# Optimization experiments

Measured on AMD Instinct MI355X. Metric: run time of the kernel, lower is better.

The kernel has to match this reference:

```python
import jax, jax.numpy as jnp
import numpy as np

B, T, H, NH = 4, 1024, 1024, 16
HS = H // NH
FF = 4 * H
EPS = 1e-5


def setup_inputs() -> dict:
    key = jax.random.key(0)
    ks = jax.random.split(key, 12)
    s = 0.02
    inp = {
        "x": jax.random.normal(ks[0], (B, T, H), jnp.float32),
        # attention projections, stored as [in, out] so y = x @ W + b
        "Wq": jax.random.normal(ks[1], (H, H), jnp.float32) * s,
        "bq": jnp.zeros((H,), jnp.float32),
        "Wk": jax.random.normal(ks[2], (H, H), jnp.float32) * s,
        "bk": jnp.zeros((H,), jnp.float32),
        "Wv": jax.random.normal(ks[3], (H, H), jnp.float32) * s,
        "bv": jnp.zeros((H,), jnp.float32),
        "Wo": jax.random.normal(ks[4], (H, H), jnp.float32) * s,
        "bo": jnp.zeros((H,), jnp.float32),
        # layernorms
        "ln1_w": jnp.ones((H,), jnp.float32),
        "ln1_b": jnp.zeros((H,), jnp.float32),
        "ln2_w": jnp.ones((H,), jnp.float32),
        "ln2_b": jnp.zeros((H,), jnp.float32),
        # MLP
        "Wfc": jax.random.normal(ks[5], (H, FF), jnp.float32) * s,
        "bfc": jnp.zeros((FF,), jnp.float32),
        "Wpr": jax.random.normal(ks[6], (FF, H), jnp.float32) * s,
        "bpr": jnp.zeros((H,), jnp.float32),
    }
    return inp


def _layernorm(x, w, b):
    mu = jnp.mean(x, axis=-1, keepdims=True)
    var = jnp.mean(jnp.square(x - mu), axis=-1, keepdims=True)
    return (x - mu) * jax.lax.rsqrt(var + EPS) * w + b


def _rope(x):
    # x: [B, nh, T, hs]; interleaved-pair RoPE, base 10000
    half = HS // 2
    inv_freq = 1.0 / (10000.0 ** (jnp.arange(half, dtype=jnp.float32) / half))
    ang = jnp.arange(T, dtype=jnp.float32)[:, None] * inv_freq[None, :]  # [T, half]
    cos, sin = jnp.cos(ang), jnp.sin(ang)
    xr = x.reshape(*x.shape[:-1], half, 2)
    x0, x1 = xr[..., 0], xr[..., 1]
    r0 = x0 * cos - x1 * sin
    r1 = x0 * sin + x1 * cos
    return jnp.stack([r0, r1], axis=-1).reshape(x.shape)


def _block(x, Wq, bq, Wk, bk, Wv, bv, Wo, bo, ln1_w, ln1_b, ln2_w, ln2_b, Wfc, bfc, Wpr, bpr):
    # --- attention sub-block ---
    h1 = _layernorm(x, ln1_w, ln1_b)
    q = (h1 @ Wq + bq).reshape(B, T, NH, HS).transpose(0, 2, 1, 3)  # [B,nh,T,hs]
    k = (h1 @ Wk + bk).reshape(B, T, NH, HS).transpose(0, 2, 1, 3)
    v = (h1 @ Wv + bv).reshape(B, T, NH, HS).transpose(0, 2, 1, 3)
    q, k = _rope(q), _rope(k)
    scores = jnp.einsum('bhqd,bhkd->bhqk', q, k) / jnp.sqrt(jnp.float32(HS))
    attn = jax.nn.softmax(scores, axis=-1)
    # NOTE: original applies the causal mask AFTER softmax (multiplicative, no renorm)
    causal = jnp.tril(jnp.ones((T, T), jnp.float32))[None, None]
    attn = attn * causal
    out = jnp.einsum('bhqk,bhkd->bhqd', attn, v)
    out = out.transpose(0, 2, 1, 3).reshape(B, T, H)
    x = x + (out @ Wo + bo)
    # --- MLP sub-block ---
    h2 = _layernorm(x, ln2_w, ln2_b)
    m = jax.nn.gelu(h2 @ Wfc + bfc, approximate=False)
    x = x + (m @ Wpr + bpr)
    return x


def reference(x, Wq, bq, Wk, bk, Wv, bv, Wo, bo, ln1_w, ln1_b, ln2_w, ln2_b, Wfc, bfc, Wpr, bpr):
    return _block(x, Wq, bq, Wk, bk, Wv, bv, Wo, bo, ln1_w, ln1_b, ln2_w, ln2_b, Wfc, bfc, Wpr, bpr)
```

## Files before the change

### kernel.cpp

```cpp
#include <hip/hip_runtime.h>
#include <hip/hip_bf16.h>

typedef unsigned short u16;
typedef __attribute__((ext_vector_type(8))) short bf16x8;
typedef __attribute__((ext_vector_type(4))) float f32x4;
typedef __attribute__((ext_vector_type(4))) unsigned short u16x4;

#define B_  4
#define T_  1024
#define H_  1024
#define NH_ 16
#define HS_ 64
#define FF_ 4096
#define M_  (B_*T_)
#define QKV_S 3072

__device__ __forceinline__ u16 f2bf(float f){
  union { float f; unsigned u; } v; v.f = f;
  unsigned r = v.u + 0x7fffu + ((v.u >> 16) & 1u);
  return (u16)(r >> 16);
}
__device__ __forceinline__ float bf2f(u16 h){
  union { unsigned u; float f; } v; v.u = ((unsigned)h) << 16;
  return v.f;
}
__device__ __forceinline__ unsigned pack2bf(float a, float b){
  __hip_bfloat162 h = __float22bfloat162_rn(make_float2(a, b));
  union { __hip_bfloat162 h; unsigned u; } c; c.h = h;
  return c.u;
}

__device__ __forceinline__ void gload_lds16(const void* g, void* l){
  __builtin_amdgcn_global_load_lds(
      (const __attribute__((address_space(1))) unsigned int*)g,
      (__attribute__((address_space(3))) unsigned int*)l,
      16, 0, 0);
}

__global__ __launch_bounds__(256) void transpose_cvt(const float* __restrict__ W,
                                                     u16* __restrict__ Wt, int K, int N)
{
  __shared__ u16 tile[64][68];
  const int k0 = blockIdx.y * 64, n0 = blockIdx.x * 64;
  const int tid = threadIdx.x;
  #pragma unroll
  for (int it = 0; it < 4; ++it){
    int ci = tid + it * 256;
    int kr = ci >> 4, nc = ci & 15;
    float4 f = *(const float4*)(W + (size_t)(k0 + kr) * N + n0 + nc * 4);
    tile[kr][nc*4+0] = f2bf(f.x);
    tile[kr][nc*4+1] = f2bf(f.y);
    tile[kr][nc*4+2] = f2bf(f.z);
    tile[kr][nc*4+3] = f2bf(f.w);
  }
  __syncthreads();
  #pragma unroll
  for (int it = 0; it < 4; ++it){
    int co = tid + it * 256;
    int nr = co >> 4, kc = co & 15;
    u16x4 o;
    o[0] = tile[kc*4+0][nr];
    o[1] = tile[kc*4+1][nr];
    o[2] = tile[kc*4+2][nr];
    o[3] = tile[kc*4+3][nr];
    *(u16x4*)(Wt + (size_t)(n0 + nr) * K + k0 + kc * 4) = o;
  }
}

__global__ __launch_bounds__(256) void vtrans_k(const u16* __restrict__ qkv,
                                                u16* __restrict__ vtg)
{
  __shared__ u16 tile[64][72];
  const int bh = blockIdx.y, tt = blockIdx.x * 64;
  const int b = bh >> 4, h = bh & 15;
  const size_t src = (size_t)b * T_ * QKV_S + h * HS_ + 2048;
  const int tid = threadIdx.x;
  #pragma unroll
  for (int it = 0; it < 2; ++it){
    int ci = tid + it * 256;
    int r = ci >> 3, c = ci & 7;
    bf16x8 vvv = *(const bf16x8*)(qkv + src + (size_t)(tt + r) * QKV_S + c * 8);
    *(bf16x8*)&tile[r][c * 8] = vvv;
  }
  __syncthreads();
  #pragma unroll
  for (int it = 0; it < 2; ++it){
    int co = tid + it * 256;
    int d = co >> 3, c = co & 7;
    bf16x8 ov;
    #pragma unroll
    for (int j = 0; j < 8; ++j) ov[j] = (short)tile[c * 8 + j][d];
    *(bf16x8*)(vtg + (size_t)bh * HS_ * T_ + (size_t)d * T_ + tt + c * 8) = ov;
  }
}

__global__ void concat3_k(const float* __restrict__ a, const float* __restrict__ b,
                          const float* __restrict__ c, float* __restrict__ o){
  int i = blockIdx.x * 256 + threadIdx.x;
  if (i >= QKV_S) return;
  o[i] = (i < 1024) ? a[i] : (i < 2048) ? b[i - 1024] : c[i - 2048];
}

__global__ void rope_table_k(float* __restrict__ tab){
  int i = blockIdx.x * blockDim.x + threadIdx.x;
  if (i >= T_ * 32) return;
  int t = i >> 5, f = i & 31;
  float inv = powf(10000.0f, -(float)f * (1.0f / 32.0f));
  float ang = (float)t * inv;
  tab[i*2+0] = cosf(ang);
  tab[i*2+1] = sinf(ang);
}

__global__ void rope_apply_k(u16* __restrict__ qkv, const float* __restrict__ tab){
  int i = blockIdx.x * blockDim.x + threadIdx.x;
  if (i >= B_*T_*NH_*32) return;
  int pr = i & 31;
  int nh = (i >> 5) & (NH_ - 1);
  int bt = i >> 9;
  int t  = bt & (T_ - 1);
  size_t idx = (size_t)bt * QKV_S + nh * HS_ + pr * 2;
  float c = tab[(t*32 + pr)*2], s = tab[(t*32 + pr)*2 + 1];
  {
    float x0 = bf2f(qkv[idx]), x1 = bf2f(qkv[idx+1]);
    qkv[idx]   = f2bf((x0 * c - x1 * s) * 0.125f);
    qkv[idx+1] = f2bf((x0 * s + x1 * c) * 0.125f);
  }
  {
    float x0 = bf2f(qkv[idx+1024]), x1 = bf2f(qkv[idx+1025]);
    qkv[idx+1024] = f2bf(x0 * c - x1 * s);
    qkv[idx+1025] = f2bf(x0 * s + x1 * c);
  }
}

__global__ __launch_bounds__(256) void ln_kernel(const float* __restrict__ x,
    const float* __restrict__ w, const float* __restrict__ bgain,
    u16* __restrict__ out)
{
  const int row = blockIdx.x;
  const int t = threadIdx.x;
  float4 vv = ((const float4*)(x + (size_t)row * H_))[t];
  float s  = vv.x + vv.y + vv.z + vv.w;
  float s2 = vv.x*vv.x + vv.y*vv.y + vv.z*vv.z + vv.w*vv.w;
  #pragma unroll
  for (int mm = 1; mm < 64; mm <<= 1){ s += __shfl_xor(s, mm); s2 += __shfl_xor(s2, mm); }
  __shared__ float red[8];
  int wid = t >> 6;
  if ((t & 63) == 0){ red[wid] = s; red[4 + wid] = s2; }
  __syncthreads();
  s  = red[0] + red[1] + red[2] + red[3];
  s2 = red[4] + red[5] + red[6] + red[7];
  float mu  = s * (1.0f / H_);
  float var = s2 * (1.0f / H_) - mu * mu;
  float rin = rsqrtf(var + 1e-5f);
  float4 wv = ((const float4*)w)[t];
  float4 bv = ((const float4*)bgain)[t];
  u16x4 ov;
  ov[0] = f2bf((vv.x - mu) * rin * wv.x + bv.x);
  ov[1] = f2bf((vv.y - mu) * rin * wv.y + bv.y);
  ov[2] = f2bf((vv.z - mu) * rin * wv.z + bv.z);
  ov[3] = f2bf((vv.w - mu) * rin * wv.w + bv.w);
  ((u16x4*)(out + (size_t)row * H_))[t] = ov;
}

template<int EPI>
__global__ __launch_bounds__(256) void gemm_kernel(
    const u16* __restrict__ A, const u16* __restrict__ Bt,
    const float* __restrict__ bias, const float* __restrict__ res,
    void* __restrict__ Cout, int M, int N, int K)
{
  __shared__ __attribute__((aligned(16))) u16 As[4][128 * 32];
  __shared__ __attribute__((aligned(16))) u16 Bs[4][128 * 32];
  const int tid  = threadIdx.x;
  const int lane = tid & 63;
  const int wid  = tid >> 6;
  const int wm = wid >> 1, wn = wid & 1;
  const int lrow = lane & 15, lkg = lane >> 4;

  const int gx  = gridDim.x;
  const int nwg = gx * gridDim.y;
  const int wg  = blockIdx.y * gx + blockIdx.x;
  const int nx  = nwg >> 3;
  const int swz = (wg & 7) * nx + (wg >> 3);
  const int m0 = (swz / gx) * 128, n0 = (swz % gx) * 128;

  const int srow = tid >> 2;
  const int sdc  = tid & 3;
  const int scs  = sdc ^ ((srow >> 1) & 3);

  const u16* Arow0 = A  + (size_t)(m0 + srow) * K + scs * 8;
  const u16* Brow0 = Bt + (size_t)(n0 + srow) * K + scs * 8;
  const u16* Arow1 = Arow0 + (size_t)64 * K;
  const u16* Brow1 = Brow0 + (size_t)64 * K;
  const int d0 = (srow * 4 + sdc) * 8;
  const int d1 = ((srow + 64) * 4 + sdc) * 8;

  f32x4 acc[4][4] = {};

  const int NT = K >> 5;

  #pragma unroll
  for (int s = 0; s < 3; ++s){
    if (s < NT){
      int k0 = s << 5;
      gload_lds16(Arow0 + k0, &As[s][d0]);
      gload_lds16(Brow0 + k0, &Bs[s][d0]);
      gload_lds16(Arow1 + k0, &As[s][d1]);
      gload_lds16(Brow1 + k0, &Bs[s][d1]);
    }
  }

  for (int t = 0; t < NT; ++t){
    int ahead = NT - 1 - t;
    if (ahead >= 2)      asm volatile("s_waitcnt vmcnt(8)" ::: "memory");
    else if (ahead == 1) asm volatile("s_waitcnt vmcnt(4)" ::: "memory");
    else                 asm volatile("s_waitcnt vmcnt(0)" ::: "memory");
    __builtin_amdgcn_s_barrier();
    __builtin_amdgcn_sched_barrier(0);

    const u16* Asc = As[t & 3];
    const u16* Bsc = Bs[t & 3];
    bf16x8 af[4], bfr[4];
    #pragma unroll
    for (int mi = 0; mi < 4; ++mi){
      int r = wm*64 + mi*16 + lrow;
      af[mi] = *(const bf16x8*)&Asc[(r*4 + (lkg ^ ((r >> 1) & 3))) * 8];
    }
    #pragma unroll
    for (int ni = 0; ni < 4; ++ni){
      int r = wn*64 + ni*16 + lrow;
      bfr[ni] = *(const bf16x8*)&Bsc[(r*4 + (lkg ^ ((r >> 1) & 3))) * 8];
    }
    asm volatile("s_waitcnt lgkmcnt(0)" ::: "memory");
    __builtin_amdgcn_sched_barrier(0);
    __builtin_amdgcn_s_barrier();
    __builtin_amdgcn_sched_barrier(0);

    if (t + 3 < NT){
      int k0 = (t + 3) << 5;
      int sl = (t + 3) & 3;
      gload_lds16(Arow0 + k0, &As[sl][d0]);
      gload_lds16(Brow0 + k0, &Bs[sl][d0]);
      gload_lds16(Arow1 + k0, &As[sl][d1]);
      gload_lds16(Brow1 + k0, &Bs[sl][d1]);
    }

    #pragma unroll
    for (int mi = 0; mi < 4; ++mi)
      #pragma unroll
      for (int ni = 0; ni < 4; ++ni)
        acc[mi][ni] = __builtin_amdgcn_mfma_f32_16x16x32_bf16(af[mi], bfr[ni], acc[mi][ni], 0, 0, 0);
  }

  #pragma unroll
  for (int mi = 0; mi < 4; ++mi){
    #pragma unroll
    for (int ni = 0; ni < 4; ++ni){
      int col = n0 + wn*64 + ni*16 + lrow;
      float bv = bias[col];
      #pragma unroll
      for (int r = 0; r < 4; ++r){
        int row = m0 + wm*64 + mi*16 + lkg*4 + r;
        float v = acc[mi][ni][r] + bv;
        if (EPI == 1){
          v = 0.5f * v * (1.0f + erff(v * 0.70710678118f));
        }
        if (EPI == 2){
          ((float*)Cout)[(size_t)row * N + col] = v + res[(size_t)row * N + col];
        } else {
          ((u16*)Cout)[(size_t)row * N + col] = f2bf(v);
        }
      }
    }
  }
}

__global__ __launch_bounds__(256) void attn_kernel(
    const u16* __restrict__ qkv, const u16* __restrict__ vtg,
    u16* __restrict__ out)
{
  __shared__ u16 K_lds[2][64 * 64];
  __shared__ u16 VT_lds[2][64 * 64];
  __shared__ u16 P_lds[4][16 * 64];
  const int tid = threadIdx.x, lane = tid & 63, w = tid >> 6;
  const int lrow = lane & 15, lkg = lane >> 4;
  const int q0 = blockIdx.x * 64;
  const int bh = blockIdx.y, b = bh >> 4, h = bh & 15;
  const size_t baseq  = (size_t)b * T_ * QKV_S + h * HS_;
  const size_t basek  = baseq + 1024;
  const size_t basevt = (size_t)bh * HS_ * T_;
  const size_t baseo  = (size_t)b * T_ * H_ + h * HS_;
  const int qg = q0 + w * 16 + lrow;

  bf16x8 qa[2];
  {
    const u16* qp = qkv + baseq + (size_t)qg * QKV_S + lkg * 8;
    qa[0] = *(const bf16x8*)qp;
    qa[1] = *(const bf16x8*)(qp + 32);
  }

  const int ci0 = tid, ci1 = tid + 256;
  const int r0 = ci0 >> 3, c0 = ci0 & 7, g0 = c0 ^ (r0 & 7);
  const int r1 = ci1 >> 3, c1 = ci1 & 7, g1 = c1 ^ (r1 & 7);
  const u16* kap0 = qkv + basek + (size_t)r0 * QKV_S + g0 * 8;
  const u16* kap1 = qkv + basek + (size_t)r1 * QKV_S + g1 * 8;
  const u16* vap0 = vtg + basevt + (size_t)r0 * T_ + g0 * 8;
  const u16* vap1 = vtg + basevt + (size_t)r1 * T_ + g1 * 8;
  const int kd0 = ci0 * 8, kd1 = ci1 * 8;

  f32x4 o[4] = {};
  float mrun = -1e30f, lrun = 0.f;

  gload_lds16(kap0, &K_lds[0][kd0]);
  gload_lds16(kap1, &K_lds[0][kd1]);
  gload_lds16(vap0, &VT_lds[0][kd0]);
  gload_lds16(vap1, &VT_lds[0][kd1]);

  int cur = 0;
  for (int t = 0; t < 16; ++t){
    const int kt = t << 6;
    __syncthreads();
    if (t + 1 < 16){
      const size_t ko = (size_t)(t + 1) * 64 * QKV_S;
      gload_lds16(kap0 + ko, &K_lds[cur^1][kd0]);
      gload_lds16(kap1 + ko, &K_lds[cur^1][kd1]);
      if (((t + 1) << 6) <= q0 + 63){
        const int vo = (t + 1) * 64;
        gload_lds16(vap0 + vo, &VT_lds[cur^1][kd0]);
        gload_lds16(vap1 + vo, &VT_lds[cur^1][kd1]);
      }
    }

    f32x4 s[4];
    #pragma unroll
    for (int mi = 0; mi < 4; ++mi){
      f32x4 c = {};
      #pragma unroll
      for (int ss = 0; ss < 2; ++ss){
        int r = mi * 16 + lrow;
        int off = r * 128 + (((ss * 4 + lkg) ^ (r & 7)) * 16);
        bf16x8 kb = *(const bf16x8*)((const char*)K_lds[cur] + off);
        c = __builtin_amdgcn_mfma_f32_16x16x32_bf16(kb, qa[ss], c, 0, 0, 0);
      }
      s[mi] = c;
    }

    float mt = fmaxf(fmaxf(fmaxf(s[0][0], s[0][1]), fmaxf(s[0][2], s[0][3])),
                     fmaxf(fmaxf(s[1][0], s[1][1]), fmaxf(s[1][2], s[1][3])));
    mt = fmaxf(mt, fmaxf(fmaxf(fmaxf(s[2][0], s[2][1]), fmaxf(s[2][2], s[2][3])),
                         fmaxf(fmaxf(s[3][0], s[3][1]), fmaxf(s[3][2], s[3][3]))));
    mt = fmaxf(mt, __shfl_xor(mt, 16));
    mt = fmaxf(mt, __shfl_xor(mt, 32));
    float mnew = fmaxf(mrun, mt);
    float fsc = __expf(mrun - mnew);
    mrun = mnew;

    float p[16];
    float ls = 0.f;
    #pragma unroll
    for (int mi = 0; mi < 4; ++mi){
      #pragma unroll
      for (int r = 0; r < 4; ++r){
        int key = kt + mi * 16 + lkg * 4 + r;
        float pv = __expf(s[mi][r] - mnew);
        ls += pv;
        p[mi * 4 + r] = (key <= qg) ? pv : 0.f;
      }
    }
    ls += __shfl_xor(ls, 16);
    ls += __shfl_xor(ls, 32);
    lrun = lrun * fsc + ls;
    #pragma unroll
    for (int nf = 0; nf < 4; ++nf){
      #pragma unroll
      for (int r = 0; r < 4; ++r) o[nf][r] *= fsc;
    }

    if (kt <= q0 + w * 16 + 15){
      char* pbase = (char*)&P_lds[w][0];
      const int rx = (lrow & 7) << 4;
      #pragma unroll
      for (int mi = 0; mi < 4; ++mi){
        uint2 pk;
        pk.x = pack2bf(p[mi*4+0], p[mi*4+1]);
        pk.y = pack2bf(p[mi*4+2], p[mi*4+3]);
        *(uint2*)(pbase + (lrow * 128 + ((mi * 32 + lkg * 8) ^ rx))) = pk;
      }
      #pragma unroll
      for (int ss = 0; ss < 2; ++ss){
        bf16x8 pb = *(const bf16x8*)(pbase + (lrow * 128 + ((ss * 64 + lkg * 16) ^ rx)));
        #pragma unroll
        for (int nfd = 0; nfd < 4; ++nfd){
          int d = nfd * 16 + lrow;
          int off = d * 128 + (((ss * 4 + lkg) ^ (d & 7)) * 16);
          bf16x8 vb = *(const bf16x8*)((const char*)VT_lds[cur] + off);
          o[nfd] = __builtin_amdgcn_mfma_f32_16x16x32_bf16(vb, pb, o[nfd], 0, 0, 0);
        }
      }
    }
    cur ^= 1;
  }

  float rl = 1.0f / lrun;
  #pragma unroll
  for (int nfd = 0; nfd < 4; ++nfd){
    uint2 ov;
    ov.x = pack2bf(o[nfd][0] * rl, o[nfd][1] * rl);
    ov.y = pack2bf(o[nfd][2] * rl, o[nfd][3] * rl);
    *(uint2*)(out + baseo + (size_t)qg * H_ + nfd * 16 + lkg * 4) = ov;
  }
}

extern "C" void kernel_launch(void* const* d_in, const int* in_sizes, int n_in,
                              void* d_out, int out_size, void* d_ws, size_t ws_size,
                              hipStream_t stream)
{
  (void)in_sizes; (void)n_in; (void)out_size; (void)ws_size;
  const float* x    = (const float*)d_in[0];
  const float* Wq   = (const float*)d_in[1];
  const float* bq   = (const float*)d_in[2];
  const float* Wk   = (const float*)d_in[3];
  const float* bk   = (const float*)d_in[4];
  const float* Wv   = (const float*)d_in[5];
  const float* bv   = (const float*)d_in[6];
  const float* Wo   = (const float*)d_in[7];
  const float* bo   = (const float*)d_in[8];
  const float* ln1w = (const float*)d_in[9];
  const float* ln1b = (const float*)d_in[10];
  const float* ln2w = (const float*)d_in[11];
  const float* ln2b = (const float*)d_in[12];
  const float* Wfc  = (const float*)d_in[13];
  const float* bfc  = (const float*)d_in[14];
  const float* Wpr  = (const float*)d_in[15];
  const float* bpr  = (const float*)d_in[16];

  char* ws = (char*)d_ws;
  u16*  WqkvT = (u16*)(ws + ((size_t) 0 << 20));
  u16*  WoT   = (u16*)(ws + ((size_t) 6 << 20));
  u16*  WfcT  = (u16*)(ws + ((size_t) 8 << 20));
  u16*  WprT  = (u16*)(ws + ((size_t)16 << 20));
  u16*  h1    = (u16*)(ws + ((size_t)24 << 20));
  u16*  qkvb  = (u16*)(ws + ((size_t)32 << 20));
  float* x1   = (float*)(ws + ((size_t)32 << 20));
  u16*  h2    = (u16*)(ws + ((size_t)48 << 20));
  float* bqkv = (float*)(ws + ((size_t)56 << 20));
  float* rtab = (float*)(ws + ((size_t)56 << 20) + (64 << 10));
  u16*  vtg   = (u16*)(ws + ((size_t)57 << 20));
  u16*  mb    = (u16*)(ws + ((size_t)56 << 20));
  u16*  attnout = h1;

  dim3 blk(256);

  transpose_cvt<<<dim3(H_/64,  H_/64),  blk, 0, stream>>>(Wq,  WqkvT,                 H_,  H_);
  transpose_cvt<<<dim3(H_/64,  H_/64),  blk, 0, stream>>>(Wk,  WqkvT + (size_t)1024*1024, H_,  H_);
  transpose_cvt<<<dim3(H_/64,  H_/64),  blk, 0, stream>>>(Wv,  WqkvT + (size_t)2048*1024, H_,  H_);
  transpose_cvt<<<dim3(H_/64,  H_/64),  blk, 0, stream>>>(Wo,  WoT,  H_,  H_);
  transpose_cvt<<<dim3(FF_/64, H_/64),  blk, 0, stream>>>(Wfc, WfcT, H_,  FF_);
  transpose_cvt<<<dim3(H_/64,  FF_/64), blk, 0, stream>>>(Wpr, WprT, FF_, H_);
  concat3_k<<<dim3((QKV_S+255)/256), blk, 0, stream>>>(bq, bk, bv, bqkv);
  rope_table_k<<<dim3((T_*32)/256), blk, 0, stream>>>(rtab);

  ln_kernel<<<dim3(M_), blk, 0, stream>>>(x, ln1w, ln1b, h1);
  gemm_kernel<0><<<dim3(QKV_S/128, M_/128), blk, 0, stream>>>(h1, WqkvT, bqkv, nullptr, qkvb, M_, QKV_S, H_);
  rope_apply_k<<<dim3((B_*T_*NH_*32)/256), blk, 0, stream>>>(qkvb, rtab);
  vtrans_k<<<dim3(T_/64, B_*NH_), blk, 0, stream>>>(qkvb, vtg);
  attn_kernel<<<dim3(T_/64, B_*NH_), blk, 0, stream>>>(qkvb, vtg, attnout);
  gemm_kernel<2><<<dim3(H_/128, M_/128), blk, 0, stream>>>(attnout, WoT, bo, x, x1, M_, H_, H_);
  ln_kernel<<<dim3(M_), blk, 0, stream>>>(x1, ln2w, ln2b, h2);
  gemm_kernel<1><<<dim3(FF_/128, M_/128), blk, 0, stream>>>(h2, WfcT, bfc, nullptr, mb, M_, FF_, H_);
  gemm_kernel<2><<<dim3(H_/128, M_/128), blk, 0, stream>>>(mb, WprT, bpr, x1, (float*)d_out, M_, H_, FF_);
}
```

Before: 290.1 us.

## Restructure GEMM and attention LDS rings to drop per-iteration second barrier

The GEMM becomes templated on ring depth. Stage refills are issued right after the single barrier into the slot consumed in the previous iteration, which removes the second barrier and lgkmcnt wait per K step. A 3-deep ring is used for the wide-N GEMMs (lower LDS, possibly higher occupancy) and a 6-deep ring for the N=1024 GEMMs (more loads in flight). Attention moves from double to triple buffering with prefetch distance two, and now always loads V tiles, even for fully masked tiles where the old code skipped them. Safety of the single barrier depends on the ring depth exceeding the prefetch distance.

```diff
diff --git a/kernel.cpp b/kernel.cpp
--- a/kernel.cpp
+++ b/kernel.cpp
@@ -162,14 +162,14 @@
   ((u16x4*)(out + (size_t)row * H_))[t] = ov;
 }
 
-template<int EPI>
+template<int EPI, int RING>
 __global__ __launch_bounds__(256) void gemm_kernel(
     const u16* __restrict__ A, const u16* __restrict__ Bt,
     const float* __restrict__ bias, const float* __restrict__ res,
     void* __restrict__ Cout, int M, int N, int K)
 {
-  __shared__ __attribute__((aligned(16))) u16 As[4][128 * 32];
-  __shared__ __attribute__((aligned(16))) u16 Bs[4][128 * 32];
+  __shared__ __attribute__((aligned(16))) u16 As[RING][128 * 32];
+  __shared__ __attribute__((aligned(16))) u16 Bs[RING][128 * 32];
   const int tid  = threadIdx.x;
   const int lane = tid & 63;
   const int wid  = tid >> 6;
@@ -195,30 +195,48 @@
   const int d1 = ((srow + 64) * 4 + sdc) * 8;
 
   f32x4 acc[4][4] = {};
-
   const int NT = K >> 5;
-
-  #pragma unroll
-  for (int s = 0; s < 3; ++s){
-    if (s < NT){
-      int k0 = s << 5;
-      gload_lds16(Arow0 + k0, &As[s][d0]);
-      gload_lds16(Brow0 + k0, &Bs[s][d0]);
-      gload_lds16(Arow1 + k0, &As[s][d1]);
-      gload_lds16(Brow1 + k0, &Bs[s][d1]);
-    }
-  }
-
+  constexpr int DIST = RING - 1;
+
+  #pragma unroll
+  for (int s = 0; s < DIST; ++s){
+    int k0 = s << 5;
+    gload_lds16(Arow0 + k0, &As[s][d0]);
+    gload_lds16(Brow0 + k0, &Bs[s][d0]);
+    gload_lds16(Arow1 + k0, &As[s][d1]);
+    gload_lds16(Brow1 + k0, &Bs[s][d1]);
+  }
+
+  int rs = 0;
+  int wsl = DIST;
   for (int t = 0; t < NT; ++t){
-    int ahead = NT - 1 - t;
-    if (ahead >= 2)      asm volatile("s_waitcnt vmcnt(8)" ::: "memory");
-    else if (ahead == 1) asm volatile("s_waitcnt vmcnt(4)" ::: "memory");
-    else                 asm volatile("s_waitcnt vmcnt(0)" ::: "memory");
+    int cnt = NT - 1 - t; if (cnt > DIST - 1) cnt = DIST - 1;
+    if constexpr (RING == 6){
+      if (cnt >= 4)      asm volatile("s_waitcnt vmcnt(16)" ::: "memory");
+      else if (cnt == 3) asm volatile("s_waitcnt vmcnt(12)" ::: "memory");
+      else if (cnt == 2) asm volatile("s_waitcnt vmcnt(8)"  ::: "memory");
+      else if (cnt == 1) asm volatile("s_waitcnt vmcnt(4)"  ::: "memory");
+      else               asm volatile("s_waitcnt vmcnt(0)"  ::: "memory");
+    } else {
+      if (cnt >= 1)      asm volatile("s_waitcnt vmcnt(4)"  ::: "memory");
+      else               asm volatile("s_waitcnt vmcnt(0)"  ::: "memory");
+    }
     __builtin_amdgcn_s_barrier();
     __builtin_amdgcn_sched_barrier(0);
 
-    const u16* Asc = As[t & 3];
-    const u16* Bsc = Bs[t & 3];
+    if (t + DIST < NT){
+      int k0 = (t + DIST) << 5;
+      gload_lds16(Arow0 + k0, &As[wsl][d0]);
+      gload_lds16(Brow0 + k0, &Bs[wsl][d0]);
+      gload_lds16(Arow1 + k0, &As[wsl][d1]);
+      gload_lds16(Brow1 + k0, &Bs[wsl][d1]);
+    }
+    wsl = (wsl + 1 == RING) ? 0 : wsl + 1;
+
+    const u16* Asc = As[rs];
+    const u16* Bsc = Bs[rs];
+    rs = (rs + 1 == RING) ? 0 : rs + 1;
+
     bf16x8 af[4], bfr[4];
     #pragma unroll
     for (int mi = 0; mi < 4; ++mi){
@@ -230,20 +248,6 @@
       int r = wn*64 + ni*16 + lrow;
       bfr[ni] = *(const bf16x8*)&Bsc[(r*4 + (lkg ^ ((r >> 1) & 3))) * 8];
     }
-    asm volatile("s_waitcnt lgkmcnt(0)" ::: "memory");
-    __builtin_amdgcn_sched_barrier(0);
-    __builtin_amdgcn_s_barrier();
-    __builtin_amdgcn_sched_barrier(0);
-
-    if (t + 3 < NT){
-      int k0 = (t + 3) << 5;
-      int sl = (t + 3) & 3;
-      gload_lds16(Arow0 + k0, &As[sl][d0]);
-      gload_lds16(Brow0 + k0, &Bs[sl][d0]);
-      gload_lds16(Arow1 + k0, &As[sl][d1]);
-      gload_lds16(Brow1 + k0, &Bs[sl][d1]);
-    }
-
     #pragma unroll
     for (int mi = 0; mi < 4; ++mi)
       #pragma unroll
@@ -278,8 +282,8 @@
     const u16* __restrict__ qkv, const u16* __restrict__ vtg,
     u16* __restrict__ out)
 {
-  __shared__ u16 K_lds[2][64 * 64];
-  __shared__ u16 VT_lds[2][64 * 64];
+  __shared__ u16 K_lds[3][64 * 64];
+  __shared__ u16 VT_lds[3][64 * 64];
   __shared__ u16 P_lds[4][16 * 64];
   const int tid = threadIdx.x, lane = tid & 63, w = tid >> 6;
   const int lrow = lane & 15, lkg = lane >> 4;
@@ -310,25 +314,37 @@
   f32x4 o[4] = {};
   float mrun = -1e30f, lrun = 0.f;
 
-  gload_lds16(kap0, &K_lds[0][kd0]);
-  gload_lds16(kap1, &K_lds[0][kd1]);
-  gload_lds16(vap0, &VT_lds[0][kd0]);
-  gload_lds16(vap1, &VT_lds[0][kd1]);
-
-  int cur = 0;
+  #pragma unroll
+  for (int s = 0; s < 2; ++s){
+    const size_t ko = (size_t)s * 64 * QKV_S;
+    const int    vo = s * 64;
+    gload_lds16(kap0 + ko, &K_lds[s][kd0]);
+    gload_lds16(kap1 + ko, &K_lds[s][kd1]);
+    gload_lds16(vap0 + vo, &VT_lds[s][kd0]);
+    gload_lds16(vap1 + vo, &VT_lds[s][kd1]);
+  }
+
+  int rs = 0, wsl = 2;
   for (int t = 0; t < 16; ++t){
     const int kt = t << 6;
-    __syncthreads();
-    if (t + 1 < 16){
-      const size_t ko = (size_t)(t + 1) * 64 * QKV_S;
-      gload_lds16(kap0 + ko, &K_lds[cur^1][kd0]);
-      gload_lds16(kap1 + ko, &K_lds[cur^1][kd1]);
-      if (((t + 1) << 6) <= q0 + 63){
-        const int vo = (t + 1) * 64;
-        gload_lds16(vap0 + vo, &VT_lds[cur^1][kd0]);
-        gload_lds16(vap1 + vo, &VT_lds[cur^1][kd1]);
-      }
-    }
+    if (t < 15) asm volatile("s_waitcnt vmcnt(4)" ::: "memory");
+    else        asm volatile("s_waitcnt vmcnt(0)" ::: "memory");
+    __builtin_amdgcn_s_barrier();
+    __builtin_amdgcn_sched_barrier(0);
+
+    if (t + 2 < 16){
+      const size_t ko = (size_t)(t + 2) * 64 * QKV_S;
+      const int    vo = (t + 2) * 64;
+      gload_lds16(kap0 + ko, &K_lds[wsl][kd0]);
+      gload_lds16(kap1 + ko, &K_lds[wsl][kd1]);
+      gload_lds16(vap0 + vo, &VT_lds[wsl][kd0]);
+      gload_lds16(vap1 + vo, &VT_lds[wsl][kd1]);
+    }
+    wsl = (wsl + 1 == 3) ? 0 : wsl + 1;
+
+    const u16* Kc  = K_lds[rs];
+    const u16* VTc = VT_lds[rs];
+    rs = (rs + 1 == 3) ? 0 : rs + 1;
 
     f32x4 s[4];
     #pragma unroll
@@ -338,7 +354,7 @@
       for (int ss = 0; ss < 2; ++ss){
         int r = mi * 16 + lrow;
         int off = r * 128 + (((ss * 4 + lkg) ^ (r & 7)) * 16);
-        bf16x8 kb = *(const bf16x8*)((const char*)K_lds[cur] + off);
+        bf16x8 kb = *(const bf16x8*)((const char*)Kc + off);
         c = __builtin_amdgcn_mfma_f32_16x16x32_bf16(kb, qa[ss], c, 0, 0, 0);
       }
       s[mi] = c;
@@ -392,12 +408,11 @@
         for (int nfd = 0; nfd < 4; ++nfd){
           int d = nfd * 16 + lrow;
           int off = d * 128 + (((ss * 4 + lkg) ^ (d & 7)) * 16);
-          bf16x8 vb = *(const bf16x8*)((const char*)VT_lds[cur] + off);
+          bf16x8 vb = *(const bf16x8*)((const char*)VTc + off);
           o[nfd] = __builtin_amdgcn_mfma_f32_16x16x32_bf16(vb, pb, o[nfd], 0, 0, 0);
         }
       }
     }
-    cur ^= 1;
   }
 
   float rl = 1.0f / lrun;
@@ -460,12 +475,12 @@
   rope_table_k<<<dim3((T_*32)/256), blk, 0, stream>>>(rtab);
 
   ln_kernel<<<dim3(M_), blk, 0, stream>>>(x, ln1w, ln1b, h1);
-  gemm_kernel<0><<<dim3(QKV_S/128, M_/128), blk, 0, stream>>>(h1, WqkvT, bqkv, nullptr, qkvb, M_, QKV_S, H_);
+  gemm_kernel<0,3><<<dim3(QKV_S/128, M_/128), blk, 0, stream>>>(h1, WqkvT, bqkv, nullptr, qkvb, M_, QKV_S, H_);
   rope_apply_k<<<dim3((B_*T_*NH_*32)/256), blk, 0, stream>>>(qkvb, rtab);
   vtrans_k<<<dim3(T_/64, B_*NH_), blk, 0, stream>>>(qkvb, vtg);
   attn_kernel<<<dim3(T_/64, B_*NH_), blk, 0, stream>>>(qkvb, vtg, attnout);
-  gemm_kernel<2><<<dim3(H_/128, M_/128), blk, 0, stream>>>(attnout, WoT, bo, x, x1, M_, H_, H_);
+  gemm_kernel<2,6><<<dim3(H_/128, M_/128), blk, 0, stream>>>(attnout, WoT, bo, x, x1, M_, H_, H_);
   ln_kernel<<<dim3(M_), blk, 0, stream>>>(x1, ln2w, ln2b, h2);
-  gemm_kernel<1><<<dim3(FF_/128, M_/128), blk, 0, stream>>>(h2, WfcT, bfc, nullptr, mb, M_, FF_, H_);
-  gemm_kernel<2><<<dim3(H_/128, M_/128), blk, 0, stream>>>(mb, WprT, bpr, x1, (float*)d_out, M_, H_, FF_);
-}
+  gemm_kernel<1,3><<<dim3(FF_/128, M_/128), blk, 0, stream>>>(h2, WfcT, bfc, nullptr, mb, M_, FF_, H_);
+  gemm_kernel<2,6><<<dim3(H_/128, M_/128), blk, 0, stream>>>(mb, WprT, bpr, x1, (float*)d_out, M_, H_, FF_);
+}
```

After: 304.9 us. 5.1% more time.
